# Performance work log

Measured on AMD Instinct MI355X. Metric: run time of the kernel, lower is better.

## Reference

```python
import jax, jax.numpy as jnp
import numpy as np

B, N, C = 4, 2048, 768
H, QK_R, VP_R = 12, 32, 32  # heads, per-head q/k rank, per-head v rank
HEAD_DIM = 64               # original head_dim -> scale = head_dim ** -0.5


def setup_inputs() -> dict:
    key = jax.random.key(0)
    kx, kq, kk, kv, kp = jax.random.split(key, 5)
    s = lambda fan_in: 1.0 / np.sqrt(fan_in)
    return {
        "x": jax.random.normal(kx, (B, N, C), dtype=jnp.float32),
        "Wq": jax.random.normal(kq, (C, H * QK_R), dtype=jnp.float32) * s(C),
        "Wk": jax.random.normal(kk, (C, H * QK_R), dtype=jnp.float32) * s(C),
        "Wv": jax.random.normal(kv, (C, H * VP_R), dtype=jnp.float32) * s(C),
        "Wp": jax.random.normal(kp, (H * VP_R, C), dtype=jnp.float32) * s(H * VP_R),
    }


def reference(x, Wq, Wk, Wv, Wp):
    b, n, c = x.shape
    scale = HEAD_DIM ** -0.5
    # low-rank projections, split per head: [B, H, N, r]
    q = (x @ Wq).reshape(b, n, H, QK_R).transpose(0, 2, 1, 3)
    k = (x @ Wk).reshape(b, n, H, QK_R).transpose(0, 2, 1, 3)
    v = (x @ Wv).reshape(b, n, H, VP_R).transpose(0, 2, 1, 3)
    attn = jnp.einsum("bhnr,bhmr->bhnm", q, k) * scale  # [B, H, N, N]
    attn = jax.nn.softmax(attn, axis=-1)                 # attn_drop rate 0 -> identity
    out = jnp.einsum("bhnm,bhmr->bhnr", attn, v)        # [B, H, N, VP_R]
    out = out.transpose(0, 2, 1, 3).reshape(b, n, H * VP_R)
    return out @ Wp                                      # proj_drop rate 0 -> identity
```

## Files before the change

kernel.cpp:

```cpp
#include <hip/hip_runtime.h>
#include <hip/hip_bf16.h>
#include <stdint.h>
#include <math.h>

#define B_   4
#define N_   2048
#define C_   768
#define H_   12
#define R_   32
#define M_   (B_ * N_)
#define QKV_ (H_ * R_)

#define QSCALE 0.18033688011112042f

#define KST 40
#define VST 136

typedef __attribute__((ext_vector_type(8))) short    bf16x8;
typedef __attribute__((ext_vector_type(4))) float    f32x4;
typedef __attribute__((ext_vector_type(8))) unsigned short u16x8;
typedef __attribute__((ext_vector_type(4))) _Float16 f16x4;

#if defined(__has_builtin)
#if __has_builtin(__builtin_amdgcn_exp2f)
#define EXP2F(x) __builtin_amdgcn_exp2f(x)
#else
#define EXP2F(x) exp2f(x)
#endif
#else
#define EXP2F(x) exp2f(x)
#endif

__device__ __forceinline__ short f2bf(float f) {
    union { float f; uint32_t u; } v; v.f = f;
    uint32_t u = v.u;
    uint32_t r = (u + 0x7fffu + ((u >> 16) & 1u)) >> 16;
    return (short)r;
}

__device__ __forceinline__ uint32_t packbf2(float a, float b) {
    __hip_bfloat162 h = __float22bfloat162_rn(float2{a, b});
    uint32_t u; __builtin_memcpy(&u, &h, 4); return u;
}

__device__ __forceinline__ uint32_t packh2(float a, float b) {
    auto h = __builtin_amdgcn_cvt_pkrtz(a, b);
    uint32_t u; __builtin_memcpy(&u, &h, 4); return u;
}

__device__ __forceinline__ void gll16(const short* g, short* l) {
    __builtin_amdgcn_global_load_lds(
        (const __attribute__((address_space(1))) uint32_t*)g,
        (__attribute__((address_space(3))) uint32_t*)l, 16, 0, 0);
}

__global__ __launch_bounds__(256) void prep(
    const float* __restrict__ X,
    const float* __restrict__ Wq, const float* __restrict__ Wk,
    const float* __restrict__ Wv, const float* __restrict__ Wp,
    short* __restrict__ wts, short* __restrict__ wpt, short* __restrict__ Xb) {
    int bid = blockIdx.x;
    if (bid < 288) {
        __shared__ short Ls[64 * 65];
        int z = bid / 72;
        int t = bid - z * 72;
        const float* src; float scl; short* dst; int trt, tct, Psrc, Pdst;
        if (z < 3) {
            trt = t / 6; tct = t - (t / 6) * 6;
            Psrc = 384; Pdst = 768;
            src = (z == 0) ? Wq : (z == 1) ? Wk : Wv;
            scl = (z == 0) ? QSCALE : 1.0f;
            dst = wts + (size_t)z * (QKV_ * C_);
        } else {
            trt = t / 12; tct = t - (t / 12) * 12;
            Psrc = 768; Pdst = 384;
            src = Wp; scl = 1.0f; dst = wpt;
        }
        int r0 = trt * 64, c0 = tct * 64;
        int rr = threadIdx.x >> 2;
        int cc = (threadIdx.x & 3) * 16;
        const float4* s4 = (const float4*)(src + (size_t)(r0 + rr) * Psrc + c0 + cc);
        float4 f0 = s4[0], f1 = s4[1], f2 = s4[2], f3 = s4[3];
        short* lp = &Ls[rr * 65 + cc];
        lp[0]=f2bf(f0.x*scl); lp[1]=f2bf(f0.y*scl); lp[2]=f2bf(f0.z*scl); lp[3]=f2bf(f0.w*scl);
        lp[4]=f2bf(f1.x*scl); lp[5]=f2bf(f1.y*scl); lp[6]=f2bf(f1.z*scl); lp[7]=f2bf(f1.w*scl);
        lp[8]=f2bf(f2.x*scl); lp[9]=f2bf(f2.y*scl); lp[10]=f2bf(f2.z*scl); lp[11]=f2bf(f2.w*scl);
        lp[12]=f2bf(f3.x*scl); lp[13]=f2bf(f3.y*scl); lp[14]=f2bf(f3.z*scl); lp[15]=f2bf(f3.w*scl);
        __syncthreads();
        int jr = threadIdx.x >> 2;
        int seg = (threadIdx.x & 3) * 16;
        u16x8 o0, o1;
        #pragma unroll
        for (int u = 0; u < 8; u++) {
            o0[u] = (unsigned short)Ls[(seg + u) * 65 + jr];
            o1[u] = (unsigned short)Ls[(seg + 8 + u) * 65 + jr];
        }
        short* dp = dst + (size_t)(c0 + jr) * Pdst + r0 + seg;
        *(u16x8*)dp = o0;
        *(u16x8*)(dp + 8) = o1;
    } else {
        size_t i = ((size_t)(bid - 288) * 256 + threadIdx.x) * 8;
        const float4* s4 = (const float4*)(X + i);
        float4 f0 = s4[0], f1 = s4[1];
        u16x8 o;
        o[0]=f2bf(f0.x); o[1]=f2bf(f0.y); o[2]=f2bf(f0.z); o[3]=f2bf(f0.w);
        o[4]=f2bf(f1.x); o[5]=f2bf(f1.y); o[6]=f2bf(f1.z); o[7]=f2bf(f1.w);
        *(u16x8*)(Xb + i) = o;
    }
}

__global__ __launch_bounds__(256, 3) void qkv_gemm(
    const short* __restrict__ Xb, const short* __restrict__ wts,
    short* __restrict__ qkvout) {
    const int mt = blockIdx.x, nt = blockIdx.y;
    const int m0 = mt * 128, j0 = nt * 128;
    const int z = nt / 3;

    __shared__ short smem[2 * 128 * 64];
    short* As = smem;
    short* Bs = smem + 128 * 64;
    short* Tt = smem;

    const int tid = threadIdx.x;
    const int lane = tid & 63, w = tid >> 6;
    const int l16 = lane & 15, quad = lane >> 4;
    const int wm = w & 1, wn = w >> 1;

    const int srow = w * 32 + (lane >> 3);
    const int scol = (((lane & 7) ^ (lane >> 3))) * 8;
    const short* pa = Xb  + (size_t)(m0 + srow) * C_ + scol;
    const short* pb = wts + (size_t)(j0 + srow) * C_ + scol;

    f32x4 acc[4][4] = {};

    for (int k0 = 0; k0 < C_; k0 += 64) {
        __syncthreads();
        #pragma unroll
        for (int j = 0; j < 4; j++) {
            gll16(pa + (size_t)j * 8 * C_ + k0, &As[(w * 32 + j * 8) * 64]);
            gll16(pb + (size_t)j * 8 * C_ + k0, &Bs[(w * 32 + j * 8) * 64]);
        }
        __syncthreads();
        #pragma unroll
        for (int ks = 0; ks < 2; ks++) {
            bf16x8 af[4], bf[4];
            #pragma unroll
            for (int i = 0; i < 4; i++) {
                int ar = wm * 64 + i * 16 + l16;
                af[i] = *(const bf16x8*)&As[ar * 64 + (((ks * 4 + quad) ^ (ar & 7)) * 8)];
                int br = wn * 64 + i * 16 + l16;
                bf[i] = *(const bf16x8*)&Bs[br * 64 + (((ks * 4 + quad) ^ (br & 7)) * 8)];
            }
            #pragma unroll
            for (int i = 0; i < 4; i++)
                #pragma unroll
                for (int c = 0; c < 4; c++)
                    acc[i][c] = __builtin_amdgcn_mfma_f32_16x16x32_bf16(af[i], bf[c], acc[i][c], 0, 0, 0);
        }
    }

    const size_t S = (size_t)B_ * H_ * N_ * R_;
    if (z < 2) {
        #pragma unroll
        for (int c = 0; c < 4; c++) {
            int j = j0 + wn * 64 + c * 16 + l16;
            int zz = j / 384;
            int jz = j - zz * 384;
            int h = jz >> 5, r = jz & 31;
            short* outz = qkvout + (size_t)zz * S;
            #pragma unroll
            for (int i = 0; i < 4; i++) {
                #pragma unroll
                for (int reg = 0; reg < 4; reg++) {
                    int m = m0 + wm * 64 + i * 16 + quad * 4 + reg;
                    int bb = m >> 11, n = m & (N_ - 1);
                    outz[(((size_t)(bb * H_ + h)) * N_ + n) * R_ + r] = f2bf(acc[i][c][reg]);
                }
            }
        }
    } else {
        const int bb = m0 >> 11;
        const int nl0 = m0 & (N_ - 1);
        short* vout = qkvout + 2 * S;
        #pragma unroll
        for (int p = 0; p < 2; p++) {
            __syncthreads();
            if (wn == p) {
                #pragma unroll
                for (int i = 0; i < 4; i++)
                    #pragma unroll
                    for (int c = 0; c < 4; c++) {
                        uint32_t d0 = packh2(acc[i][c][0], acc[i][c][1]);
                        uint32_t d1 = packh2(acc[i][c][2], acc[i][c][3]);
                        uint2 dd = {d0, d1};
                        *(uint2*)&Tt[(c * 16 + l16) * 132 + wm * 64 + i * 16 + quad * 4] = dd;
                    }
            }
            __syncthreads();
            int jr = tid >> 2;
            int seg = (tid & 3) * 32;
            int jz = (nt - 6) * 128 + p * 64 + jr;
            int hh = jz >> 5, rr = jz & 31;
            short* dst = vout + (((size_t)(bb * H_ + hh)) * R_ + rr) * N_ + nl0 + seg;
            #pragma unroll
            for (int q4 = 0; q4 < 4; q4++) {
                u16x8 vv = *(const u16x8*)&Tt[jr * 132 + seg + q4 * 8];
                *(u16x8*)(dst + q4 * 8) = vv;
            }
        }
    }
}

__global__ __launch_bounds__(256, 3) void attn(
    const short* __restrict__ qkv, short* __restrict__ O) {
    const int qt = blockIdx.x, h = blockIdx.y, b = blockIdx.z;
    const size_t S = (size_t)B_ * H_ * N_ * R_;
    const short* Q  = qkv + ((size_t)(b * H_ + h)) * N_ * R_;
    const short* K  = qkv + S + ((size_t)(b * H_ + h)) * N_ * R_;
    const short* Vt = qkv + 2 * S + ((size_t)(b * H_ + h)) * R_ * N_;

    __shared__ short Ks[2][128 * KST];
    __shared__ short Vs[2][32 * VST];

    const int tid = threadIdx.x;
    const int lane = tid & 63, wave = tid >> 6;
    const int l16 = lane & 15, quad = lane >> 4;

    bf16x8 aq[2];
    #pragma unroll
    for (int g = 0; g < 2; g++)
        aq[g] = *(const bf16x8*)(Q + (size_t)(qt * 128 + wave * 32 + g * 16 + l16) * R_ + quad * 8);

    f16x4 onesh;
    #pragma unroll
    for (int j = 0; j < 4; j++) onesh[j] = (_Float16)1.0f;

    f32x4 o0T[2] = {}, o1T[2] = {}, lacc[2] = {};

    const int krow = tid >> 1;
    const int khalf = (tid & 1) * 16;
    const short* kgp = K + (size_t)krow * R_ + khalf;
    const int kwoff = krow * KST + khalf;
    const int vrow = tid >> 3;
    const int vcol = (tid & 7) * 16;
    const short* vgp = Vt + (size_t)vrow * N_ + vcol;
    const int vwoff = vrow * VST + vcol;

    {
        u16x8 ka = *(const u16x8*)kgp;
        u16x8 kb2 = *(const u16x8*)(kgp + 8);
        u16x8 va = *(const u16x8*)vgp;
        u16x8 vb2 = *(const u16x8*)(vgp + 8);
        *(u16x8*)&Ks[0][kwoff]     = ka;
        *(u16x8*)&Ks[0][kwoff + 8] = kb2;
        *(u16x8*)&Vs[0][vwoff]     = va;
        *(u16x8*)&Vs[0][vwoff + 8] = vb2;
    }
    __syncthreads();

    for (int it = 0; it < 16; ++it) {
        const int kt0 = it * 128;
        const int cur = it & 1;
        u16x8 kn0, kn1, vn0, vn1;
        if (it < 15) {
            kn0 = *(const u16x8*)(kgp + (size_t)(kt0 + 128) * R_);
            kn1 = *(const u16x8*)(kgp + (size_t)(kt0 + 128) * R_ + 8);
            vn0 = *(const u16x8*)(vgp + kt0 + 128);
            vn1 = *(const u16x8*)(vgp + kt0 + 128 + 8);
        }

        bf16x8 kf[8];
        #pragma unroll
        for (int c = 0; c < 8; c++)
            kf[c] = *(const bf16x8*)&Ks[cur][(c * 16 + l16) * KST + quad * 8];

        #pragma unroll
        for (int c = 0; c < 8; c++) {
            f16x4 v0 = *(const f16x4*)&Vs[cur][l16 * VST + c * 16 + quad * 4];
            f16x4 v1 = *(const f16x4*)&Vs[cur][(16 + l16) * VST + c * 16 + quad * 4];
            #pragma unroll
            for (int g = 0; g < 2; g++) {
                f32x4 zz = {};
                f32x4 sT = __builtin_amdgcn_mfma_f32_16x16x32_bf16(kf[c], aq[g], zz, 0, 0, 0);
                union { f16x4 v; uint32_t w[2]; } pu;
                pu.w[0] = packh2(EXP2F(sT[0]), EXP2F(sT[1]));
                pu.w[1] = packh2(EXP2F(sT[2]), EXP2F(sT[3]));
                f16x4 pf = pu.v;
                o0T[g]  = __builtin_amdgcn_mfma_f32_16x16x16f16(v0, pf, o0T[g], 0, 0, 0);
                o1T[g]  = __builtin_amdgcn_mfma_f32_16x16x16f16(v1, pf, o1T[g], 0, 0, 0);
                lacc[g] = __builtin_amdgcn_mfma_f32_16x16x16f16(onesh, pf, lacc[g], 0, 0, 0);
            }
        }

        if (it < 15) {
            *(u16x8*)&Ks[cur ^ 1][kwoff]     = kn0;
            *(u16x8*)&Ks[cur ^ 1][kwoff + 8] = kn1;
            *(u16x8*)&Vs[cur ^ 1][vwoff]     = vn0;
            *(u16x8*)&Vs[cur ^ 1][vwoff + 8] = vn1;
        }
        __syncthreads();
    }

    #pragma unroll
    for (int g = 0; g < 2; g++) {
        float inv = 1.0f / lacc[g][0];
        int n = qt * 128 + wave * 32 + g * 16 + l16;
        size_t base = ((size_t)b * N_ + n) * QKV_ + h * R_;
        uint32_t a0 = packbf2(o0T[g][0] * inv, o0T[g][1] * inv);
        uint32_t a1 = packbf2(o0T[g][2] * inv, o0T[g][3] * inv);
        uint2 s0 = {a0, a1};
        *(uint2*)&O[base + quad * 4] = s0;
        uint32_t b0 = packbf2(o1T[g][0] * inv, o1T[g][1] * inv);
        uint32_t b1 = packbf2(o1T[g][2] * inv, o1T[g][3] * inv);
        uint2 s1 = {b0, b1};
        *(uint2*)&O[base + 16 + quad * 4] = s1;
    }
}

__global__ __launch_bounds__(256, 3) void out_gemm(
    const short* __restrict__ Ob, const short* __restrict__ wpt,
    float* __restrict__ out) {
    const int mt = blockIdx.x, nt = blockIdx.y;
    const int m0 = mt * 128, j0 = nt * 64;

    __shared__ short As[128 * 64];
    __shared__ short Bs[64 * 64];

    const int tid = threadIdx.x;
    const int lane = tid & 63, w = tid >> 6;
    const int l16 = lane & 15, quad = lane >> 4;

    const int sarow = w * 32 + (lane >> 3);
    const int sbrow = w * 16 + (lane >> 3);
    const int scol = (((lane & 7) ^ (lane >> 3))) * 8;
    const short* pa = Ob  + (size_t)(m0 + sarow) * QKV_ + scol;
    const short* pb = wpt + (size_t)(j0 + sbrow) * QKV_ + scol;

    f32x4 acc[2][4] = {};

    for (int k0 = 0; k0 < QKV_; k0 += 64) {
        __syncthreads();
        #pragma unroll
        for (int j = 0; j < 4; j++)
            gll16(pa + (size_t)j * 8 * QKV_ + k0, &As[(w * 32 + j * 8) * 64]);
        #pragma unroll
        for (int j = 0; j < 2; j++)
            gll16(pb + (size_t)j * 8 * QKV_ + k0, &Bs[(w * 16 + j * 8) * 64]);
        __syncthreads();
        #pragma unroll
        for (int ks = 0; ks < 2; ks++) {
            bf16x8 af[2], bf[4];
            #pragma unroll
            for (int i = 0; i < 2; i++) {
                int ar = w * 32 + i * 16 + l16;
                af[i] = *(const bf16x8*)&As[ar * 64 + (((ks * 4 + quad) ^ (ar & 7)) * 8)];
            }
            #pragma unroll
            for (int c = 0; c < 4; c++) {
                int br = c * 16 + l16;
                bf[c] = *(const bf16x8*)&Bs[br * 64 + (((ks * 4 + quad) ^ (br & 7)) * 8)];
            }
            #pragma unroll
            for (int i = 0; i < 2; i++)
                #pragma unroll
                for (int c = 0; c < 4; c++)
                    acc[i][c] = __builtin_amdgcn_mfma_f32_16x16x32_bf16(af[i], bf[c], acc[i][c], 0, 0, 0);
        }
    }

    #pragma unroll
    for (int i = 0; i < 2; i++)
        #pragma unroll
        for (int c = 0; c < 4; c++)
            #pragma unroll
            for (int reg = 0; reg < 4; reg++) {
                int m = m0 + w * 32 + i * 16 + quad * 4 + reg;
                out[(size_t)m * C_ + j0 + c * 16 + l16] = acc[i][c][reg];
            }
}

extern "C" void kernel_launch(void* const* d_in, const int* in_sizes, int n_in,
                              void* d_out, int out_size, void* d_ws, size_t ws_size,
                              hipStream_t stream) {
    const float* x  = (const float*)d_in[0];
    const float* Wq = (const float*)d_in[1];
    const float* Wk = (const float*)d_in[2];
    const float* Wv = (const float*)d_in[3];
    const float* Wp = (const float*)d_in[4];
    float* out = (float*)d_out;

    short* ws16 = (short*)d_ws;
    short* wts  = ws16;
    short* wpt  = wts + (size_t)3 * QKV_ * C_;
    short* qkv  = wpt + (size_t)QKV_ * C_;
    short* Obuf = qkv + (size_t)3 * B_ * H_ * N_ * R_;
    short* Xb   = Obuf + (size_t)B_ * N_ * QKV_;

    prep<<<dim3(288 + 3072), 256, 0, stream>>>(x, Wq, Wk, Wv, Wp, wts, wpt, Xb);
    qkv_gemm<<<dim3(M_ / 128, (3 * QKV_) / 128), 256, 0, stream>>>(Xb, wts, qkv);
    attn<<<dim3(N_ / 128, H_, B_), 256, 0, stream>>>(qkv, Obuf);
    out_gemm<<<dim3(M_ / 128, C_ / 64), 256, 0, stream>>>(Obuf, wpt, out);
}
```

Baseline: 152.0 us.

## Split attention key tiles across two wave groups with LDS reduction

The attention kernel now runs 512 threads per block. Two groups of four waves each process half of every 128-key tile for the same 128 queries, then combine their partial outputs and row sums through shared memory before normalizing and storing. Each thread now loads half as much K/V per tile. The aim is more waves in flight to hide exp and MFMA latency, since the grid only has 768 blocks. The cost is an extra LDS reduction, a barrier, and tighter register pressure under launch_bounds(512,6).

```diff
diff --git a/kernel.cpp b/kernel.cpp
--- a/kernel.cpp
+++ b/kernel.cpp
@@ -211,7 +211,7 @@
     }
 }
 
-__global__ __launch_bounds__(256, 3) void attn(
+__global__ __launch_bounds__(512, 6) void attn(
     const short* __restrict__ qkv, short* __restrict__ O) {
     const int qt = blockIdx.x, h = blockIdx.y, b = blockIdx.z;
     const size_t S = (size_t)B_ * H_ * N_ * R_;
@@ -219,17 +219,19 @@
     const short* K  = qkv + S + ((size_t)(b * H_ + h)) * N_ * R_;
     const short* Vt = qkv + 2 * S + ((size_t)(b * H_ + h)) * R_ * N_;
 
-    __shared__ short Ks[2][128 * KST];
-    __shared__ short Vs[2][32 * VST];
+    __shared__ short sbuf[2 * 128 * KST + 2 * 32 * VST];
+    short* Ksb = sbuf;
+    short* Vsb = sbuf + 2 * 128 * KST;
 
     const int tid = threadIdx.x;
     const int lane = tid & 63, wave = tid >> 6;
+    const int wq = wave & 3, wk = wave >> 2;
     const int l16 = lane & 15, quad = lane >> 4;
 
     bf16x8 aq[2];
     #pragma unroll
     for (int g = 0; g < 2; g++)
-        aq[g] = *(const bf16x8*)(Q + (size_t)(qt * 128 + wave * 32 + g * 16 + l16) * R_ + quad * 8);
+        aq[g] = *(const bf16x8*)(Q + (size_t)(qt * 128 + wq * 32 + g * 16 + l16) * R_ + quad * 8);
 
     f16x4 onesh;
     #pragma unroll
@@ -237,47 +239,45 @@
 
     f32x4 o0T[2] = {}, o1T[2] = {}, lacc[2] = {};
 
-    const int krow = tid >> 1;
-    const int khalf = (tid & 1) * 16;
-    const short* kgp = K + (size_t)krow * R_ + khalf;
-    const int kwoff = krow * KST + khalf;
-    const int vrow = tid >> 3;
-    const int vcol = (tid & 7) * 16;
+    const int krow = tid >> 2;
+    const int kseg = (tid & 3) * 8;
+    const short* kgp = K + (size_t)krow * R_ + kseg;
+    const int kwoff = krow * KST + kseg;
+    const int vrow = tid >> 4;
+    const int vcol = (tid & 15) * 8;
     const short* vgp = Vt + (size_t)vrow * N_ + vcol;
     const int vwoff = vrow * VST + vcol;
 
     {
         u16x8 ka = *(const u16x8*)kgp;
-        u16x8 kb2 = *(const u16x8*)(kgp + 8);
         u16x8 va = *(const u16x8*)vgp;
-        u16x8 vb2 = *(const u16x8*)(vgp + 8);
-        *(u16x8*)&Ks[0][kwoff]     = ka;
-        *(u16x8*)&Ks[0][kwoff + 8] = kb2;
-        *(u16x8*)&Vs[0][vwoff]     = va;
-        *(u16x8*)&Vs[0][vwoff + 8] = vb2;
+        *(u16x8*)&Ksb[kwoff] = ka;
+        *(u16x8*)&Vsb[vwoff] = va;
     }
     __syncthreads();
 
     for (int it = 0; it < 16; ++it) {
         const int kt0 = it * 128;
         const int cur = it & 1;
-        u16x8 kn0, kn1, vn0, vn1;
+        u16x8 kn, vn;
         if (it < 15) {
-            kn0 = *(const u16x8*)(kgp + (size_t)(kt0 + 128) * R_);
-            kn1 = *(const u16x8*)(kgp + (size_t)(kt0 + 128) * R_ + 8);
-            vn0 = *(const u16x8*)(vgp + kt0 + 128);
-            vn1 = *(const u16x8*)(vgp + kt0 + 128 + 8);
-        }
-
-        bf16x8 kf[8];
-        #pragma unroll
-        for (int c = 0; c < 8; c++)
-            kf[c] = *(const bf16x8*)&Ks[cur][(c * 16 + l16) * KST + quad * 8];
-
-        #pragma unroll
-        for (int c = 0; c < 8; c++) {
-            f16x4 v0 = *(const f16x4*)&Vs[cur][l16 * VST + c * 16 + quad * 4];
-            f16x4 v1 = *(const f16x4*)&Vs[cur][(16 + l16) * VST + c * 16 + quad * 4];
+            kn = *(const u16x8*)(kgp + (size_t)(kt0 + 128) * R_);
+            vn = *(const u16x8*)(vgp + kt0 + 128);
+        }
+
+        const short* Kc = &Ksb[cur * 128 * KST];
+        const short* Vc = &Vsb[cur * 32 * VST];
+
+        bf16x8 kf[4];
+        #pragma unroll
+        for (int c = 0; c < 4; c++)
+            kf[c] = *(const bf16x8*)&Kc[((wk * 4 + c) * 16 + l16) * KST + quad * 8];
+
+        #pragma unroll
+        for (int c = 0; c < 4; c++) {
+            const int cc = wk * 4 + c;
+            f16x4 v0 = *(const f16x4*)&Vc[l16 * VST + cc * 16 + quad * 4];
+            f16x4 v1 = *(const f16x4*)&Vc[(16 + l16) * VST + cc * 16 + quad * 4];
             #pragma unroll
             for (int g = 0; g < 2; g++) {
                 f32x4 zz = {};
@@ -293,27 +293,44 @@
         }
 
         if (it < 15) {
-            *(u16x8*)&Ks[cur ^ 1][kwoff]     = kn0;
-            *(u16x8*)&Ks[cur ^ 1][kwoff + 8] = kn1;
-            *(u16x8*)&Vs[cur ^ 1][vwoff]     = vn0;
-            *(u16x8*)&Vs[cur ^ 1][vwoff + 8] = vn1;
-        }
-        __syncthreads();
-    }
-
-    #pragma unroll
-    for (int g = 0; g < 2; g++) {
-        float inv = 1.0f / lacc[g][0];
-        int n = qt * 128 + wave * 32 + g * 16 + l16;
-        size_t base = ((size_t)b * N_ + n) * QKV_ + h * R_;
-        uint32_t a0 = packbf2(o0T[g][0] * inv, o0T[g][1] * inv);
-        uint32_t a1 = packbf2(o0T[g][2] * inv, o0T[g][3] * inv);
-        uint2 s0 = {a0, a1};
-        *(uint2*)&O[base + quad * 4] = s0;
-        uint32_t b0 = packbf2(o1T[g][0] * inv, o1T[g][1] * inv);
-        uint32_t b1 = packbf2(o1T[g][2] * inv, o1T[g][3] * inv);
-        uint2 s1 = {b0, b1};
-        *(uint2*)&O[base + 16 + quad * 4] = s1;
+            *(u16x8*)&Ksb[(cur ^ 1) * 128 * KST + kwoff] = kn;
+            *(u16x8*)&Vsb[(cur ^ 1) * 32 * VST + vwoff]  = vn;
+        }
+        __syncthreads();
+    }
+
+    float* sm = (float*)sbuf;
+    if (wk == 1) {
+        #pragma unroll
+        for (int g = 0; g < 2; g++) {
+            int id = (wq * 2 + g) * 64 + lane;
+            *(f32x4*)&sm[id * 4]        = o0T[g];
+            *(f32x4*)&sm[2048 + id * 4] = o1T[g];
+            sm[4096 + id] = lacc[g][0];
+        }
+    }
+    __syncthreads();
+    if (wk == 0) {
+        #pragma unroll
+        for (int g = 0; g < 2; g++) {
+            int id = (wq * 2 + g) * 64 + lane;
+            f32x4 p0 = *(const f32x4*)&sm[id * 4];
+            f32x4 p1 = *(const f32x4*)&sm[2048 + id * 4];
+            float pl = sm[4096 + id];
+            f32x4 a0 = o0T[g] + p0;
+            f32x4 a1 = o1T[g] + p1;
+            float inv = 1.0f / (lacc[g][0] + pl);
+            int n = qt * 128 + wq * 32 + g * 16 + l16;
+            size_t base = ((size_t)b * N_ + n) * QKV_ + h * R_;
+            uint32_t a0w = packbf2(a0[0] * inv, a0[1] * inv);
+            uint32_t a1w = packbf2(a0[2] * inv, a0[3] * inv);
+            uint2 s0 = {a0w, a1w};
+            *(uint2*)&O[base + quad * 4] = s0;
+            uint32_t b0w = packbf2(a1[0] * inv, a1[1] * inv);
+            uint32_t b1w = packbf2(a1[2] * inv, a1[3] * inv);
+            uint2 s1 = {b0w, b1w};
+            *(uint2*)&O[base + 16 + quad * 4] = s1;
+        }
     }
 }
 
@@ -398,6 +415,6 @@
 
     prep<<<dim3(288 + 3072), 256, 0, stream>>>(x, Wq, Wk, Wv, Wp, wts, wpt, Xb);
     qkv_gemm<<<dim3(M_ / 128, (3 * QKV_) / 128), 256, 0, stream>>>(Xb, wts, qkv);
-    attn<<<dim3(N_ / 128, H_, B_), 256, 0, stream>>>(qkv, Obuf);
+    attn<<<dim3(N_ / 128, H_, B_), 512, 0, stream>>>(qkv, Obuf);
     out_gemm<<<dim3(M_ / 128, C_ / 64), 256, 0, stream>>>(Obuf, wpt, out);
 }
```

New measurement: 155.5 us. 2.3% more time.
